# Kernel optimization log

Measured on AMD Instinct MI355X. Metric: run time of the kernel, lower is better.

Reference implementation:

```python
import jax, jax.numpy as jnp
import numpy as np


def _layernorm(x, g, b, eps=1e-5):
    mu = jnp.mean(x, axis=-1, keepdims=True)
    var = jnp.var(x, axis=-1, keepdims=True)
    return (x - mu) * jax.lax.rsqrt(var + eps) * g + b


def _forward(x_real, x_imag, dt, conv_w, conv_b, spec_re, spec_im, lam_re, lam_im,
             dt_param, sigma, noise_r, noise_i, ln_g, ln_b, W1, b1, w2, b2,
             Jg_W, Jg_b, Rg_W, Rg_b):
    B, T, C, H, W = x_real.shape
    x = x_real + 1j * x_imag  # complex field [B,T,C,H,W]

    # ---- spatial mixer: 3x3 conv applied to real/imag parts (linear op) ----
    def conv(z):
        z2 = z.reshape(B * T, C, H, W)
        y = jax.lax.conv_general_dilated(z2, conv_w, (1, 1), 'SAME',
                                         dimension_numbers=('NCHW', 'OIHW', 'NCHW'))
        return (y + conv_b[None, :, None, None]).reshape(B, T, C, H, W)
    x = x + (conv(x.real) + 1j * conv(x.imag))

    # ---- spectral mixer: pointwise complex filter in FFT domain ----
    Xf = jnp.fft.fft2(x, axes=(-2, -1), norm='ortho')
    filt = (spec_re + 1j * spec_im)[None, None]  # [1,1,C,H,W]
    x = x + jnp.fft.ifft2(Xf * filt, axes=(-2, -1), norm='ortho')

    # ---- metriplectic propagator: diagonal SSM scan in rfft2 space ----
    dt_eff = dt * jax.nn.softplus(dt_param)          # [C]
    dt_scalar = dt_eff.mean()
    xs = jnp.concatenate([x.real, x.imag], axis=0)   # [2B,T,C,H,W]; B_out=2B
    u = jnp.fft.rfft2(xs, axes=(-2, -1), norm='ortho')  # [2B,T,C,H,Wf]
    lam = -jax.nn.softplus(lam_re) + 1j * lam_im     # stable poles, [C]
    A = jnp.exp(lam * dt_eff.astype(jnp.complex64))  # [C]
    A = jnp.broadcast_to(A[None, None, :, None, None], u.shape)

    def comb(e1, e2):  # first-order linear recurrence h_t = a_t h_{t-1} + u_t
        a1, u1 = e1
        a2, u2 = e2
        return (a1 * a2, a2 * u1 + u2)
    _, h = jax.lax.associative_scan(comb, (A, u), axis=1)

    xt = jnp.fft.irfft2(h, s=(H, W), axes=(-2, -1), norm='ortho')  # [2B,T,C,H,W] real
    x_temporal = xt[:B] + 1j * xt[B:]

    noise = (noise_r + 1j * noise_i) * sigma * jnp.sqrt(dt_scalar)
    x = x + x_temporal + noise

    # ---- Port-Hamiltonian layer on real||imag channel concat ----
    xp = jnp.transpose(x, (0, 1, 3, 4, 2))                  # [B,T,H,W,C]
    xc = jnp.concatenate([xp.real, xp.imag], axis=-1)       # [B,T,H,W,2C]
    D = 2 * C
    x_in = _layernorm(xc, ln_g, ln_b)
    # grads of potential H = sum(MLP(x_in)) wrt x_in
    pot = lambda z: (jax.nn.silu(z @ W1 + b1) @ w2 + b2).sum()
    grads = jax.grad(pot)(x_in)
    M = (x_in @ Jg_W + Jg_b).reshape(*xc.shape[:-1], D, D)
    Jm = M - jnp.swapaxes(M, -1, -2)
    P = (x_in @ Rg_W + Rg_b).reshape(*xc.shape[:-1], D, D)
    R = jnp.einsum('...ki,...kj->...ij', P, P) + 1e-4 * jnp.eye(D, dtype=xc.dtype)
    update = jnp.einsum('...ij,...j->...i', Jm - R, grads)
    x_ph = xc + update * dt_scalar

    # output: [B,T,2C,H,W]; real half = out.real, imag half = out.imag
    return jnp.transpose(x_ph, (0, 1, 4, 2, 3))


def setup_inputs() -> dict:
    key = jax.random.key(0)
    ks = jax.random.split(key, 16)
    B, T, C, H, W = 2, 8, 16, 64, 64
    D = 2 * C
    hid = D * 4
    f32 = jnp.float32
    rn = lambda k, s, sc=1.0: jax.random.normal(k, s, f32) * sc
    return dict(
        x_real=rn(ks[0], (B, T, C, H, W)),
        x_imag=rn(ks[1], (B, T, C, H, W)),
        dt=jnp.asarray(0.1, f32),
        conv_w=rn(ks[2], (C, C, 3, 3), 0.05),
        conv_b=jnp.zeros((C,), f32),
        spec_re=rn(ks[3], (C, H, W), 0.1),
        spec_im=rn(ks[4], (C, H, W), 0.1),
        lam_re=rn(ks[5], (C,)),
        lam_im=rn(ks[6], (C,)),
        dt_param=rn(ks[7], (C,)),
        sigma=jnp.asarray(0.01, f32),
        noise_r=rn(ks[8], (B, T, C, H, W)),
        noise_i=rn(ks[9], (B, T, C, H, W)),
        ln_g=jnp.ones((D,), f32),
        ln_b=jnp.zeros((D,), f32),
        W1=rn(ks[10], (D, hid), 0.1),
        b1=jnp.zeros((hid,), f32),
        w2=rn(ks[11], (hid,), 0.1),
        b2=jnp.asarray(0.0, f32),
        Jg_W=rn(ks[12], (D, D * D), 0.02),
        Jg_b=jnp.zeros((D * D,), f32),
        Rg_W=rn(ks[13], (D, D * D), 0.02),
        Rg_b=jnp.zeros((D * D,), f32),
    )


def reference(x_real, x_imag, dt, conv_w, conv_b, spec_re, spec_im, lam_re, lam_im,
              dt_param, sigma, noise_r, noise_i, ln_g, ln_b, W1, b1, w2, b2,
              Jg_W, Jg_b, Rg_W, Rg_b):
    return _forward(x_real, x_imag, dt, conv_w, conv_b, spec_re, spec_im, lam_re,
                    lam_im, dt_param, sigma, noise_r, noise_i, ln_g, ln_b, W1, b1,
                    w2, b2, Jg_W, Jg_b, Rg_W, Rg_b)
```

## Files before the change

### kernel.cpp

```cpp
#include <hip/hip_runtime.h>
#include <math.h>

#define Bb 2
#define Tt 8
#define Cc 16
#define Hh 64
#define Ww 64
#define Dd 32
#define HID 128
#define NPIX 4096
#define NIMG 256

typedef unsigned short ushort_t;
typedef unsigned int uint_t;
typedef __attribute__((ext_vector_type(8))) short short8;
typedef __attribute__((ext_vector_type(4))) float f32x4;
union U16 { uint4 u; short8 s; };

__device__ __forceinline__ float sp_f(float x) {
    return (x > 20.f) ? x : log1pf(expf(x));
}

__device__ __forceinline__ ushort_t f2bf(float f) {
    uint_t u = __float_as_uint(f);
    uint_t r = (u + 0x7fffu + ((u >> 16) & 1u)) >> 16;
    return (ushort_t)r;
}
__device__ __forceinline__ float bf2f(ushort_t h) { return __uint_as_float(((uint_t)h) << 16); }

__device__ __forceinline__ uint_t packbf(float hi, float lo) {
    return __builtin_amdgcn_perm(__float_as_uint(hi), __float_as_uint(lo), 0x07060302u);
}
__device__ __forceinline__ uint4 synth8(const float* gf, float xs) {
    uint4 r;
    r.x = packbf(gf[1] * xs, gf[0] * xs);
    r.y = packbf(gf[3] * xs, gf[2] * xs);
    r.z = packbf(gf[5] * xs, gf[4] * xs);
    r.w = packbf(gf[7] * xs, gf[6] * xs);
    return r;
}
__device__ __forceinline__ void expand8(uint4 v, float* f) {
    f[0] = __uint_as_float(v.x << 16); f[1] = __uint_as_float(v.x & 0xffff0000u);
    f[2] = __uint_as_float(v.y << 16); f[3] = __uint_as_float(v.y & 0xffff0000u);
    f[4] = __uint_as_float(v.z << 16); f[5] = __uint_as_float(v.z & 0xffff0000u);
    f[6] = __uint_as_float(v.w << 16); f[7] = __uint_as_float(v.w & 0xffff0000u);
}

#define MFMA16(a, b, c) __builtin_amdgcn_mfma_f32_16x16x32_bf16((a), (b), (c), 0, 0, 0)

struct cpx { float r, i; };
__device__ __forceinline__ cpx cadd(cpx a, cpx b) { return {a.r + b.r, a.i + b.i}; }
__device__ __forceinline__ cpx csub(cpx a, cpx b) { return {a.r - b.r, a.i - b.i}; }
__device__ __forceinline__ cpx cmulw(cpx a, float wr, float wi) {
    return {a.r * wr - a.i * wi, a.r * wi + a.i * wr};
}
template<int S>
__device__ __forceinline__ cpx cmulSi(cpx a) {
    return {-(float)S * a.i, (float)S * a.r};
}
template<int S>
__device__ __forceinline__ void dft8(cpx* y) {
    const float C = 0.70710678118654752f;
    cpx t0 = cadd(y[0], y[4]), t1 = csub(y[0], y[4]);
    cpx t2 = cadd(y[2], y[6]), t3 = csub(y[2], y[6]);
    cpx e0 = cadd(t0, t2), e2 = csub(t0, t2);
    cpx t3i = cmulSi<S>(t3);
    cpx e1 = cadd(t1, t3i), e3 = csub(t1, t3i);
    cpx u0 = cadd(y[1], y[5]), u1 = csub(y[1], y[5]);
    cpx u2 = cadd(y[3], y[7]), u3 = csub(y[3], y[7]);
    cpx o0 = cadd(u0, u2), o2 = csub(u0, u2);
    cpx u3i = cmulSi<S>(u3);
    cpx o1 = cadd(u1, u3i), o3 = csub(u1, u3i);
    o1 = cmulw(o1, C, (float)S * C);
    o2 = cmulSi<S>(o2);
    o3 = cmulw(o3, -C, (float)S * C);
    y[0] = cadd(e0, o0); y[4] = csub(e0, o0);
    y[1] = cadd(e1, o1); y[5] = csub(e1, o1);
    y[2] = cadd(e2, o2); y[6] = csub(e2, o2);
    y[3] = cadd(e3, o3); y[7] = csub(e3, o3);
}

template<int S>
__device__ __forceinline__ void fft2d_r8(float* reM, float* imM,
                                         const float* twr, const float* twi, int tid) {
    int j = tid & 63, g = tid >> 6;
    {
        cpx y[8];
        #pragma unroll
        for (int n1 = 0; n1 < 8; ++n1) {
            int a = j * 65 + n1 * 8 + g;
            y[n1] = {reM[a], imM[a]};
        }
        dft8<S>(y);
        #pragma unroll
        for (int k1 = 0; k1 < 8; ++k1) {
            int m = (g * k1) & 63;
            cpx b = cmulw(y[k1], twr[m], twi[m]);
            int a = j * 65 + k1 * 8 + g;
            reM[a] = b.r; imM[a] = b.i;
        }
    }
    __syncthreads();
    {
        cpx y[8];
        #pragma unroll
        for (int n2 = 0; n2 < 8; ++n2) {
            int a = j * 65 + g * 8 + n2;
            y[n2] = {reM[a], imM[a]};
        }
        dft8<S>(y);
        __syncthreads();
        #pragma unroll
        for (int k2 = 0; k2 < 8; ++k2) {
            int a = j * 65 + g + k2 * 8;
            reM[a] = y[k2].r; imM[a] = y[k2].i;
        }
    }
    __syncthreads();
    {
        cpx y[8];
        #pragma unroll
        for (int n1 = 0; n1 < 8; ++n1) {
            int a = (n1 * 8 + g) * 65 + j;
            y[n1] = {reM[a], imM[a]};
        }
        dft8<S>(y);
        #pragma unroll
        for (int k1 = 0; k1 < 8; ++k1) {
            int m = (g * k1) & 63;
            cpx b = cmulw(y[k1], twr[m], twi[m]);
            int a = (k1 * 8 + g) * 65 + j;
            reM[a] = b.r; imM[a] = b.i;
        }
    }
    __syncthreads();
    {
        cpx y[8];
        #pragma unroll
        for (int n2 = 0; n2 < 8; ++n2) {
            int a = (g * 8 + n2) * 65 + j;
            y[n2] = {reM[a], imM[a]};
        }
        dft8<S>(y);
        __syncthreads();
        #pragma unroll
        for (int k2 = 0; k2 < 8; ++k2) {
            int a = (g + k2 * 8) * 65 + j;
            reM[a] = y[k2].r; imM[a] = y[k2].i;
        }
    }
    __syncthreads();
}

__global__ __launch_bounds__(256)
void k_conv(const float* __restrict__ xr, const float* __restrict__ xi,
            const float* __restrict__ cw, const float* __restrict__ cb,
            float2* __restrict__ x1,
            const float* __restrict__ JW, const float* __restrict__ Jb,
            const float* __restrict__ RW, const float* __restrict__ Rb,
            const float* __restrict__ W1, const float* __restrict__ dtp,
            const float* __restrict__ dt_param,
            ushort_t* __restrict__ B1f, ushort_t* __restrict__ B2f,
            ushort_t* __restrict__ w1n, ushort_t* __restrict__ w1t,
            float* __restrict__ dts_out) {
    __shared__ float sre[Cc][18][18];
    __shared__ float sim[Cc][18][18];
    __shared__ float swt[8 * 16 * 12];
    __shared__ float sb[8];
    int tid = threadIdx.x;
    if (blockIdx.x >= 512) {
        const int N1 = 33 * 3072, N2 = 33 * 1024, N3 = 4096;
        int i = (blockIdx.x - 512) * 256 + tid;
        for (; i < N1 + N2 + N3; i += 40 * 256) {
            if (i < N1) {
                int s = i / 3072; int r = i % 3072;
                int ch = r >> 9; int lane = (r >> 3) & 63; int e = i & 7;
                int n = ch * 16 + (lane & 15);
                int k = s * 32 + ((lane >> 4) << 3) + e;
                float v;
                if (k < 1024) {
                    int d = k >> 5, rr = k & 31;
                    if (n < 32)      v = JW[d * 1024 + n * 32 + rr];
                    else if (n < 64) v = JW[d * 1024 + rr * 32 + (n - 32)];
                    else             v = RW[d * 1024 + (n - 64) * 32 + rr];
                } else {
                    int rr = k - 1024;
                    if (n < 32)      v = Jb[n * 32 + rr];
                    else if (n < 64) v = Jb[rr * 32 + (n - 32)];
                    else             v = Rb[(n - 64) * 32 + rr];
                }
                B1f[i] = f2bf(v);
            } else if (i < N1 + N2) {
                int i2 = i - N1;
                int s = i2 / 1024; int r = i2 % 1024;
                int ch = r >> 9; int lane = (r >> 3) & 63; int e = i2 & 7;
                int n = ch * 16 + (lane & 15);
                int k = s * 32 + ((lane >> 4) << 3) + e;
                float v;
                if (k < 1024) {
                    int d = k >> 5, kk = k & 31;
                    v = RW[d * 1024 + kk * 32 + n];
                } else {
                    v = Rb[(k - 1024) * 32 + n];
                }
                B2f[i2] = f2bf(v);
            } else {
                int i3 = i - N1 - N2;
                int d = i3 >> 7, h = i3 & 127;
                ushort_t v = f2bf(W1[i3]);
                w1n[i3] = v;
                w1t[h * 32 + d] = v;
            }
        }
        if (blockIdx.x == 512 && tid == 0) {
            float s = 0.f;
            for (int c = 0; c < Cc; ++c) s += sp_f(dt_param[c]);
            dts_out[0] = dtp[0] * s * (1.f / Cc);
        }
        return;
    }
    int blk = blockIdx.x;
    int bt = blk >> 5;
    int sub = blk & 31;
    int tile = sub >> 1, cohalf = sub & 1;
    int ty0 = (tile >> 2) * 16, tx0 = (tile & 3) * 16;
    for (int i = tid; i < 8 * 16 * 9; i += 256) {
        int g = i / 9, k = i % 9;
        swt[g * 12 + k] = cw[cohalf * 8 * 144 + i];
    }
    if (tid < 8) sb[tid] = cb[cohalf * 8 + tid];
    for (int i = tid; i < Cc * 18 * 18; i += 256) {
        int ci = i / 324; int r = i % 324; int y = r / 18, x = r % 18;
        int gy = ty0 + y - 1, gx = tx0 + x - 1;
        float vr = 0.f, vi = 0.f;
        if (gy >= 0 && gy < Hh && gx >= 0 && gx < Ww) {
            int gidx = (bt * Cc + ci) * NPIX + gy * Ww + gx;
            vr = xr[gidx]; vi = xi[gidx];
        }
        sre[ci][y][x] = vr; sim[ci][y][x] = vi;
    }
    __syncthreads();
    int py = tid >> 4, px = tid & 15;
    int gy = ty0 + py, gx = tx0 + px;
    float ar[8], ai[8];
    #pragma unroll
    for (int oc = 0; oc < 8; ++oc) {
        int cg = cohalf * 8 + oc;
        ar[oc] = sre[cg][py + 1][px + 1] + sb[oc];
        ai[oc] = sim[cg][py + 1][px + 1] + sb[oc];
    }
    for (int ci = 0; ci < Cc; ++ci) {
        float nr[9], ni[9];
        #pragma unroll
        for (int dy = 0; dy < 3; ++dy)
            #pragma unroll
            for (int dx = 0; dx < 3; ++dx) {
                nr[dy * 3 + dx] = sre[ci][py + dy][px + dx];
                ni[dy * 3 + dx] = sim[ci][py + dy][px + dx];
            }
        #pragma unroll
        for (int oc = 0; oc < 8; ++oc) {
            const float* wp = &swt[(oc * 16 + ci) * 12];
            float4 w0 = *(const float4*)&wp[0];
            float4 w1 = *(const float4*)&wp[4];
            float w8 = wp[8];
            ar[oc] += w0.x * nr[0] + w0.y * nr[1] + w0.z * nr[2]
                    + w0.w * nr[3] + w1.x * nr[4] + w1.y * nr[5]
                    + w1.z * nr[6] + w1.w * nr[7] + w8 * nr[8];
            ai[oc] += w0.x * ni[0] + w0.y * ni[1] + w0.z * ni[2]
                    + w0.w * ni[3] + w1.x * ni[4] + w1.y * ni[5]
                    + w1.z * ni[6] + w1.w * ni[7] + w8 * ni[8];
        }
    }
    #pragma unroll
    for (int oc = 0; oc < 8; ++oc)
        x1[(bt * Cc + cohalf * 8 + oc) * NPIX + gy * Ww + gx] = make_float2(ar[oc], ai[oc]);
}

__global__ __launch_bounds__(512)
void k_fft_fwd(const float2* __restrict__ x1,
               const float* __restrict__ spec_re, const float* __restrict__ spec_im,
               float2* __restrict__ X2f) {
    int img = blockIdx.x;
    int c = img % Cc;
    int tid = threadIdx.x;
    __shared__ float re[64 * 65], im[64 * 65];
    __shared__ float twr[64], twi[64];
    if (tid < 64) {
        float ang = -0.098174770424681038798f * (float)tid;
        twr[tid] = cosf(ang); twi[tid] = sinf(ang);
    }
    const float2* src = x1 + (size_t)img * NPIX;
    for (int idx = tid; idx < NPIX; idx += 512) {
        int h = idx >> 6, w = idx & 63;
        float2 v = src[idx];
        re[h * 65 + w] = v.x; im[h * 65 + w] = v.y;
    }
    __syncthreads();
    fft2d_r8<-1>(re, im, twr, twi, tid);
    const float* fr = spec_re + c * NPIX;
    const float* fi = spec_im + c * NPIX;
    float2* dst = X2f + (size_t)img * NPIX;
    for (int idx = tid; idx < NPIX; idx += 512) {
        int h = idx >> 6, w = idx & 63;
        float xr_ = re[h * 65 + w], xi_ = im[h * 65 + w];
        float gr = 1.f + fr[idx], gi = fi[idx];
        dst[idx] = make_float2(xr_ * gr - xi_ * gi, xi_ * gr + xr_ * gi);
    }
}

__global__ __launch_bounds__(256)
void k_scan2(const float2* __restrict__ Z,
             const float* __restrict__ lam_re, const float* __restrict__ lam_im,
             const float* __restrict__ dt_param, const float* __restrict__ dtp,
             float2* __restrict__ S) {
    int id = blockIdx.x * 256 + threadIdx.x;
    int w = id & 63;
    int c = (id >> 12) & 15;
    int b = id >> 16;
    float dte = dtp[0] * sp_f(dt_param[c]);
    float ea = expf(-sp_f(lam_re[c]) * dte);
    float ph = lam_im[c] * dte;
    float Ar = ea * cosf(ph), Ai = ea * sinf(ph);
    if (w > 32) Ai = -Ai;
    bool sc = (w == 0) || (w == 32);
    int pix = id & (NPIX - 1);
    int base = (b * Tt * Cc + c) * NPIX + pix;
    float s1r = 0.f, s1i = 0.f, s2r = 0.f, s2i = 0.f;
    #pragma unroll
    for (int t = 0; t < Tt; ++t) {
        int idx = base + t * (Cc * NPIX);
        float2 zv = Z[idx];
        float nr = Ar * s1r - Ai * s1i + zv.x;
        float ni = Ar * s1i + Ai * s1r + zv.y;
        s1r = nr; s1i = ni;
        float zr, zi;
        if (sc) {
            nr = Ar * s2r + Ai * s2i + zv.x;
            ni = Ar * s2i - Ai * s2r + zv.y;
            s2r = nr; s2i = ni;
            zr = 0.5f * (s1r + s2r); zi = 0.5f * (s1i + s2i);
        } else { zr = s1r; zi = s1i; }
        S[idx] = make_float2(zv.x + zr, zv.y + zi);
    }
}

__global__ __launch_bounds__(512)
void k_fft_inv(const float2* __restrict__ Sp,
               const float* __restrict__ noise_r, const float* __restrict__ noise_i,
               const float* __restrict__ sigma_p, const float* __restrict__ dts_p,
               float2* __restrict__ xf) {
    int img = blockIdx.x; int tid = threadIdx.x;
    __shared__ float re[64 * 65], im[64 * 65];
    __shared__ float twr[64], twi[64];
    if (tid < 64) {
        float ang = 0.098174770424681038798f * (float)tid;
        twr[tid] = cosf(ang); twi[tid] = sinf(ang);
    }
    const float2* src = Sp + (size_t)img * NPIX;
    for (int idx = tid; idx < NPIX; idx += 512) {
        int h = idx >> 6, w = idx & 63;
        float2 v = src[idx];
        re[h * 65 + w] = v.x; im[h * 65 + w] = v.y;
    }
    __syncthreads();
    fft2d_r8<1>(re, im, twr, twi, tid);
    float ns = sigma_p[0] * sqrtf(dts_p[0]);
    const float inv = 1.f / 4096.f;
    float2* dst = xf + (size_t)img * NPIX;
    const float* nr = noise_r + (size_t)img * NPIX;
    const float* ni = noise_i + (size_t)img * NPIX;
    for (int idx = tid; idx < NPIX; idx += 512) {
        int h = idx >> 6, w = idx & 63;
        dst[idx] = make_float2(re[h * 65 + w] * inv + ns * nr[idx],
                               im[h * 65 + w] * inv + ns * ni[idx]);
    }
}

__global__ __launch_bounds__(256, 2)
void k_ph(const float2* __restrict__ field,
          const float* __restrict__ ln_g, const float* __restrict__ ln_b,
          const float* __restrict__ b1, const float* __restrict__ w2,
          const ushort_t* __restrict__ w1n, const ushort_t* __restrict__ w1t,
          const ushort_t* __restrict__ B1f, const ushort_t* __restrict__ B2f,
          const float* __restrict__ dts_p,
          float* __restrict__ out) {
    __shared__ ushort_t xin_s[128 * 40];
    __shared__ ushort_t g_s[128 * 40];
    __shared__ ushort_t pg_s[128 * 40];
    __shared__ ushort_t A_s[128 * 136];

    int tid = threadIdx.x;
    int bt = blockIdx.x >> 5;
    int pix0 = (blockIdx.x & 31) << 7;

    int p = tid & 127, half = tid >> 7;
    const float2* fbase = field + ((size_t)bt * 16) * NPIX + pix0 + p;
    float2 xv[8];
    float s1 = 0.f, s2 = 0.f;
    #pragma unroll
    for (int j = 0; j < 8; ++j) {
        xv[j] = fbase[(half * 8 + j) * NPIX];
        s1 += xv[j].x + xv[j].y;
        s2 += xv[j].x * xv[j].x + xv[j].y * xv[j].y;
    }
    float2* red = (float2*)A_s;
    red[p * 2 + half] = make_float2(s1, s2);
    __syncthreads();
    float2 r0 = red[p * 2], r1 = red[p * 2 + 1];
    float mu = (r0.x + r1.x) * 0.03125f;
    float var = (r0.y + r1.y) * 0.03125f - mu * mu;
    float rs = rsqrtf(var + 1e-5f);
    #pragma unroll
    for (int j = 0; j < 8; ++j) {
        int cf = half * 8 + j;
        xin_s[p * 40 + cf]      = f2bf((xv[j].x - mu) * rs * ln_g[cf] + ln_b[cf]);
        xin_s[p * 40 + cf + 16] = f2bf((xv[j].y - mu) * rs * ln_g[cf + 16] + ln_b[cf + 16]);
    }
    __syncthreads();

    int lane = tid & 63, wv = tid >> 6;
    int quad = lane >> 4, l15 = lane & 15;
    const f32x4 zero4 = {0.f, 0.f, 0.f, 0.f};

    int m0z = wv * 32;
    f32x4 zacc[2][8];
    #pragma unroll
    for (int mt = 0; mt < 2; ++mt)
        #pragma unroll
        for (int nt = 0; nt < 8; ++nt) zacc[mt][nt] = zero4;
    U16 az[2];
    #pragma unroll
    for (int mt = 0; mt < 2; ++mt)
        az[mt].u = *(const uint4*)&xin_s[(m0z + mt * 16 + l15) * 40 + quad * 8];
    #pragma unroll
    for (int nt = 0; nt < 8; ++nt) {
        U16 bz;
        bz.u = *(const uint4*)&w1t[(nt * 16 + l15) * 32 + quad * 8];
        zacc[0][nt] = MFMA16(az[0].s, bz.s, zacc[0][nt]);
        zacc[1][nt] = MFMA16(az[1].s, bz.s, zacc[1][nt]);
    }
    #pragma unroll
    for (int nt = 0; nt < 8; ++nt) {
        int col = nt * 16 + l15;
        float b1v = b1[col], w2v = w2[col];
        #pragma unroll
        for (int mt = 0; mt < 2; ++mt) {
            #pragma unroll
            for (int r = 0; r < 4; ++r) {
                int row = m0z + mt * 16 + quad * 4 + r;
                float z = zacc[mt][nt][r] + b1v;
                float s = 1.f / (1.f + expf(-z));
                float t = s * (1.f + z * (1.f - s)) * w2v;
                A_s[row * 136 + col] = f2bf(t);
            }
        }
    }

    f32x4 gacc[2][2];
    #pragma unroll
    for (int mt = 0; mt < 2; ++mt)
        #pragma unroll
        for (int nt = 0; nt < 2; ++nt) gacc[mt][nt] = zero4;
    #pragma unroll
    for (int q = 0; q < 4; ++q) {
        U16 ag[2];
        #pragma unroll
        for (int mt = 0; mt < 2; ++mt)
            ag[mt].u = *(const uint4*)&A_s[(m0z + mt * 16 + l15) * 136 + q * 32 + quad * 8];
        #pragma unroll
        for (int nt = 0; nt < 2; ++nt) {
            U16 bg;
            bg.u = *(const uint4*)&w1n[(nt * 16 + l15) * 128 + q * 32 + quad * 8];
            gacc[0][nt] = MFMA16(ag[0].s, bg.s, gacc[0][nt]);
            gacc[1][nt] = MFMA16(ag[1].s, bg.s, gacc[1][nt]);
        }
    }
    #pragma unroll
    for (int mt = 0; mt < 2; ++mt)
        #pragma unroll
        for (int nt = 0; nt < 2; ++nt)
            #pragma unroll
            for (int r = 0; r < 4; ++r)
                g_s[(m0z + mt * 16 + quad * 4 + r) * 40 + nt * 16 + l15] = f2bf(gacc[mt][nt][r]);
    __syncthreads();

    int mh = wv & 1, nh = wv >> 1;
    const uint4* B1v = (const uint4*)B1f;
    const uint4* B2v = (const uint4*)B2f;
    uint_t xw[4][16];
    uint4 gvp[4];
    float gf[4][8];
    #pragma unroll
    for (int mt = 0; mt < 4; ++mt) {
        int row = mh * 64 + mt * 16 + l15;
        #pragma unroll
        for (int q = 0; q < 4; ++q)
            *(uint4*)&xw[mt][q * 4] = *(const uint4*)&xin_s[row * 40 + q * 8];
        gvp[mt] = *(const uint4*)&g_s[row * 40 + quad * 8];
        expand8(gvp[mt], gf[mt]);
    }

    uint4 br[2][3];
    #pragma unroll
    for (int pf = 0; pf < 2; ++pf)
        #pragma unroll
        for (int jj = 0; jj < 3; ++jj)
            br[pf][jj] = B1v[(pf * 6 + nh + 2 * jj) * 64 + lane];
    f32x4 acc1[3][4];
    #pragma unroll
    for (int j = 0; j < 3; ++j)
        #pragma unroll
        for (int mt = 0; mt < 4; ++mt) acc1[j][mt] = zero4;
    #pragma unroll
    for (int s = 0; s < 33; ++s) {
        int cur = s & 1;
        U16 b3[3];
        b3[0].u = br[cur][0]; b3[1].u = br[cur][1]; b3[2].u = br[cur][2];
        #pragma unroll
        for (int mt = 0; mt < 4; ++mt) {
            U16 a;
            if (s < 32) {
                uint_t u = xw[mt][s >> 1];
                float xs = (s & 1) ? __uint_as_float(u & 0xffff0000u)
                                   : __uint_as_float(u << 16);
                a.u = synth8(gf[mt], xs);
            } else {
                a.u = gvp[mt];
            }
            acc1[0][mt] = MFMA16(a.s, b3[0].s, acc1[0][mt]);
            acc1[1][mt] = MFMA16(a.s, b3[1].s, acc1[1][mt]);
            acc1[2][mt] = MFMA16(a.s, b3[2].s, acc1[2][mt]);
        }
        if (s + 2 < 33) {
            #pragma unroll
            for (int jj = 0; jj < 3; ++jj)
                br[cur][jj] = B1v[((s + 2) * 6 + nh + 2 * jj) * 64 + lane];
        }
    }
    f32x4 um[4];
    #pragma unroll
    for (int mt = 0; mt < 4; ++mt) {
        um[mt] = acc1[0][mt] - acc1[1][mt];
        #pragma unroll
        for (int r = 0; r < 4; ++r)
            pg_s[(mh * 64 + mt * 16 + quad * 4 + r) * 40 + nh * 16 + l15] = f2bf(acc1[2][mt][r]);
    }
    __syncthreads();

    uint4 pgp[4];
    float pgf[4][8];
    #pragma unroll
    for (int mt = 0; mt < 4; ++mt) {
        int row = mh * 64 + mt * 16 + l15;
        pgp[mt] = *(const uint4*)&pg_s[row * 40 + quad * 8];
        expand8(pgp[mt], pgf[mt]);
    }
    uint4 br2[2];
    br2[0] = B2v[(0 * 2 + nh) * 64 + lane];
    br2[1] = B2v[(1 * 2 + nh) * 64 + lane];
    f32x4 acc2[4];
    #pragma unroll
    for (int mt = 0; mt < 4; ++mt) acc2[mt] = zero4;
    #pragma unroll
    for (int s = 0; s < 33; ++s) {
        int cur = s & 1;
        U16 b;
        b.u = br2[cur];
        #pragma unroll
        for (int mt = 0; mt < 4; ++mt) {
            U16 a;
            if (s < 32) {
                uint_t u = xw[mt][s >> 1];
                float xs = (s & 1) ? __uint_as_float(u & 0xffff0000u)
                                   : __uint_as_float(u << 16);
                a.u = synth8(pgf[mt], xs);
            } else {
                a.u = pgp[mt];
            }
            acc2[mt] = MFMA16(a.s, b.s, acc2[mt]);
        }
        if (s + 2 < 33)
            br2[cur] = B2v[((s + 2) * 2 + nh) * 64 + lane];
    }

    __syncthreads();
    float* upd = (float*)&A_s[8192];
    #pragma unroll
    for (int mt = 0; mt < 4; ++mt) {
        int col = nh * 16 + l15;
        #pragma unroll
        for (int r = 0; r < 4; ++r) {
            int row = mh * 64 + mt * 16 + quad * 4 + r;
            float gval = bf2f(g_s[row * 40 + col]);
            upd[row * 33 + col] = um[mt][r] - acc2[mt][r] - 1e-4f * gval;
        }
    }
    __syncthreads();
    float dts = dts_p[0];
    #pragma unroll
    for (int cc = 0; cc < 16; ++cc) {
        int c = half * 16 + cc;
        float2 v = fbase[cc * NPIX];
        float xcv = half ? v.y : v.x;
        out[((size_t)bt * 32 + c) * NPIX + pix0 + p] = xcv + dts * upd[p * 33 + c];
    }
}

extern "C" void kernel_launch(void* const* d_in, const int* in_sizes, int n_in,
                              void* d_out, int out_size, void* d_ws, size_t ws_size,
                              hipStream_t stream) {
    const float* x_real   = (const float*)d_in[0];
    const float* x_imag   = (const float*)d_in[1];
    const float* dt       = (const float*)d_in[2];
    const float* conv_w   = (const float*)d_in[3];
    const float* conv_b   = (const float*)d_in[4];
    const float* spec_re  = (const float*)d_in[5];
    const float* spec_im  = (const float*)d_in[6];
    const float* lam_re   = (const float*)d_in[7];
    const float* lam_im   = (const float*)d_in[8];
    const float* dt_param = (const float*)d_in[9];
    const float* sigma    = (const float*)d_in[10];
    const float* noise_r  = (const float*)d_in[11];
    const float* noise_i  = (const float*)d_in[12];
    const float* ln_g     = (const float*)d_in[13];
    const float* ln_b     = (const float*)d_in[14];
    const float* W1       = (const float*)d_in[15];
    const float* b1       = (const float*)d_in[16];
    const float* w2       = (const float*)d_in[17];
    const float* Jg_W     = (const float*)d_in[19];
    const float* Jg_b     = (const float*)d_in[20];
    const float* Rg_W     = (const float*)d_in[21];
    const float* Rg_b     = (const float*)d_in[22];

    float2* wsA = (float2*)d_ws;
    float2* wsB = wsA + 1048576;
    float2* wsS = wsB + 1048576;

    ushort_t* B1f = (ushort_t*)(wsS + 1048576);
    ushort_t* B2f = B1f + 33 * 3072;
    ushort_t* w1n = B2f + 33 * 1024;
    ushort_t* w1t = w1n + 4096;
    float*    dts = (float*)(w1t + 4096);

    k_conv<<<552, 256, 0, stream>>>(x_real, x_imag, conv_w, conv_b, wsA,
                                    Jg_W, Jg_b, Rg_W, Rg_b, W1, dt, dt_param,
                                    B1f, B2f, w1n, w1t, dts);
    k_fft_fwd<<<NIMG, 512, 0, stream>>>(wsA, spec_re, spec_im, wsB);
    k_scan2<<<512, 256, 0, stream>>>(wsB, lam_re, lam_im, dt_param, dt, wsS);
    k_fft_inv<<<NIMG, 512, 0, stream>>>(wsS, noise_r, noise_i, sigma, dts, wsA);
    k_ph<<<512, 256, 0, stream>>>(wsA, ln_g, ln_b, b1, w2, w1n, w1t, B1f, B2f, dts,
                                  (float*)d_out);
}
```

Measured before the change: 201.0 us.

## Repartition PH bilinear GEMMs so each wave owns rows and all output columns

Changes the work split in the port-Hamiltonian kernel's bilinear MFMA stages. Each wave now owns 32 pixel rows and computes all six B1 column chunks (and both B2 chunks), where before a 2x2 split gave each wave 64 rows and half the columns. The A-operand synthesis per wave is halved, x values are read per step from LDS instead of held in a large register array, and the compile-time unroll is done with an integer_sequence helper. The cost is that every wave streams the full B1/B2 weights from global memory, doubling weight traffic per wave. An added barrier after the A_s writes makes the reuse of shared memory safe.

```diff
diff --git a/kernel.cpp b/kernel.cpp
--- a/kernel.cpp
+++ b/kernel.cpp
@@ -1,5 +1,6 @@
 #include <hip/hip_runtime.h>
 #include <math.h>
+#include <utility>
 
 #define Bb 2
 #define Tt 8
@@ -44,6 +45,15 @@
     f[2] = __uint_as_float(v.y << 16); f[3] = __uint_as_float(v.y & 0xffff0000u);
     f[4] = __uint_as_float(v.z << 16); f[5] = __uint_as_float(v.z & 0xffff0000u);
     f[6] = __uint_as_float(v.w << 16); f[7] = __uint_as_float(v.w & 0xffff0000u);
+}
+
+template <typename F, int... Is>
+__device__ __forceinline__ void unroll_impl(F&& f, std::integer_sequence<int, Is...>) {
+    (f(std::integral_constant<int, Is>{}), ...);
+}
+template <int N, typename F>
+__device__ __forceinline__ void cunroll(F&& f) {
+    unroll_impl(f, std::make_integer_sequence<int, N>{});
 }
 
 #define MFMA16(a, b, c) __builtin_amdgcn_mfma_f32_16x16x32_bf16((a), (b), (c), 0, 0, 0)
@@ -388,7 +398,7 @@
     __shared__ ushort_t xin_s[128 * 40];
     __shared__ ushort_t g_s[128 * 40];
     __shared__ ushort_t pg_s[128 * 40];
-    __shared__ ushort_t A_s[128 * 136];
+    __shared__ ushort_t A_s[128 * 136] __attribute__((aligned(16)));
 
     int tid = threadIdx.x;
     int bt = blockIdx.x >> 5;
@@ -422,8 +432,8 @@
     int lane = tid & 63, wv = tid >> 6;
     int quad = lane >> 4, l15 = lane & 15;
     const f32x4 zero4 = {0.f, 0.f, 0.f, 0.f};
-
-    int m0z = wv * 32;
+    int m0 = wv * 32;
+
     f32x4 zacc[2][8];
     #pragma unroll
     for (int mt = 0; mt < 2; ++mt)
@@ -432,7 +442,7 @@
     U16 az[2];
     #pragma unroll
     for (int mt = 0; mt < 2; ++mt)
-        az[mt].u = *(const uint4*)&xin_s[(m0z + mt * 16 + l15) * 40 + quad * 8];
+        az[mt].u = *(const uint4*)&xin_s[(m0 + mt * 16 + l15) * 40 + quad * 8];
     #pragma unroll
     for (int nt = 0; nt < 8; ++nt) {
         U16 bz;
@@ -448,7 +458,7 @@
         for (int mt = 0; mt < 2; ++mt) {
             #pragma unroll
             for (int r = 0; r < 4; ++r) {
-                int row = m0z + mt * 16 + quad * 4 + r;
+                int row = m0 + mt * 16 + quad * 4 + r;
                 float z = zacc[mt][nt][r] + b1v;
                 float s = 1.f / (1.f + expf(-z));
                 float t = s * (1.f + z * (1.f - s)) * w2v;
@@ -456,6 +466,7 @@
             }
         }
     }
+    __syncthreads();
 
     f32x4 gacc[2][2];
     #pragma unroll
@@ -467,7 +478,7 @@
         U16 ag[2];
         #pragma unroll
         for (int mt = 0; mt < 2; ++mt)
-            ag[mt].u = *(const uint4*)&A_s[(m0z + mt * 16 + l15) * 136 + q * 32 + quad * 8];
+            ag[mt].u = *(const uint4*)&A_s[(m0 + mt * 16 + l15) * 136 + q * 32 + quad * 8];
         #pragma unroll
         for (int nt = 0; nt < 2; ++nt) {
             U16 bg;
@@ -482,118 +493,113 @@
         for (int nt = 0; nt < 2; ++nt)
             #pragma unroll
             for (int r = 0; r < 4; ++r)
-                g_s[(m0z + mt * 16 + quad * 4 + r) * 40 + nt * 16 + l15] = f2bf(gacc[mt][nt][r]);
-    __syncthreads();
-
-    int mh = wv & 1, nh = wv >> 1;
+                g_s[(m0 + mt * 16 + quad * 4 + r) * 40 + nt * 16 + l15] = f2bf(gacc[mt][nt][r]);
+    __syncthreads();
+
+    const ushort_t* xr0 = &xin_s[(m0 + l15) * 40];
+    const ushort_t* xr1 = &xin_s[(m0 + 16 + l15) * 40];
+    uint4 gvp0 = *(const uint4*)&g_s[(m0 + l15) * 40 + quad * 8];
+    uint4 gvp1 = *(const uint4*)&g_s[(m0 + 16 + l15) * 40 + quad * 8];
+    float gf0[8], gf1[8];
+    expand8(gvp0, gf0);
+    expand8(gvp1, gf1);
     const uint4* B1v = (const uint4*)B1f;
     const uint4* B2v = (const uint4*)B2f;
-    uint_t xw[4][16];
-    uint4 gvp[4];
-    float gf[4][8];
-    #pragma unroll
-    for (int mt = 0; mt < 4; ++mt) {
-        int row = mh * 64 + mt * 16 + l15;
-        #pragma unroll
-        for (int q = 0; q < 4; ++q)
-            *(uint4*)&xw[mt][q * 4] = *(const uint4*)&xin_s[row * 40 + q * 8];
-        gvp[mt] = *(const uint4*)&g_s[row * 40 + quad * 8];
-        expand8(gvp[mt], gf[mt]);
-    }
-
-    uint4 br[2][3];
+
+    uint4 br[2][6];
     #pragma unroll
     for (int pf = 0; pf < 2; ++pf)
         #pragma unroll
-        for (int jj = 0; jj < 3; ++jj)
-            br[pf][jj] = B1v[(pf * 6 + nh + 2 * jj) * 64 + lane];
-    f32x4 acc1[3][4];
-    #pragma unroll
-    for (int j = 0; j < 3; ++j)
-        #pragma unroll
-        for (int mt = 0; mt < 4; ++mt) acc1[j][mt] = zero4;
-    #pragma unroll
-    for (int s = 0; s < 33; ++s) {
-        int cur = s & 1;
-        U16 b3[3];
-        b3[0].u = br[cur][0]; b3[1].u = br[cur][1]; b3[2].u = br[cur][2];
-        #pragma unroll
-        for (int mt = 0; mt < 4; ++mt) {
-            U16 a;
-            if (s < 32) {
-                uint_t u = xw[mt][s >> 1];
-                float xs = (s & 1) ? __uint_as_float(u & 0xffff0000u)
-                                   : __uint_as_float(u << 16);
-                a.u = synth8(gf[mt], xs);
-            } else {
-                a.u = gvp[mt];
+        for (int ch = 0; ch < 6; ++ch)
+            br[pf][ch] = B1v[(pf * 6 + ch) * 64 + lane];
+    f32x4 acc1[6][2];
+    #pragma unroll
+    for (int ch = 0; ch < 6; ++ch) { acc1[ch][0] = zero4; acc1[ch][1] = zero4; }
+    cunroll<33>([&](auto Sc) {
+        constexpr int s = Sc.value;
+        constexpr int cur = s & 1;
+        U16 a0, a1;
+        if constexpr (s < 32) {
+            float x0 = bf2f(xr0[s]);
+            float x1 = bf2f(xr1[s]);
+            a0.u = synth8(gf0, x0);
+            a1.u = synth8(gf1, x1);
+        } else {
+            a0.u = gvp0; a1.u = gvp1;
+        }
+        #pragma unroll
+        for (int ch = 0; ch < 6; ++ch) {
+            U16 b; b.u = br[cur][ch];
+            acc1[ch][0] = MFMA16(a0.s, b.s, acc1[ch][0]);
+            acc1[ch][1] = MFMA16(a1.s, b.s, acc1[ch][1]);
+        }
+        if constexpr (s + 2 < 33) {
+            #pragma unroll
+            for (int ch = 0; ch < 6; ++ch)
+                br[cur][ch] = B1v[((s + 2) * 6 + ch) * 64 + lane];
+        }
+    });
+    #pragma unroll
+    for (int mt = 0; mt < 2; ++mt)
+        #pragma unroll
+        for (int c2 = 0; c2 < 2; ++c2)
+            #pragma unroll
+            for (int r = 0; r < 4; ++r)
+                pg_s[(m0 + mt * 16 + quad * 4 + r) * 40 + c2 * 16 + l15] =
+                    f2bf(acc1[4 + c2][mt][r]);
+    __syncthreads();
+
+    uint4 pgp0 = *(const uint4*)&pg_s[(m0 + l15) * 40 + quad * 8];
+    uint4 pgp1 = *(const uint4*)&pg_s[(m0 + 16 + l15) * 40 + quad * 8];
+    float pgf0[8], pgf1[8];
+    expand8(pgp0, pgf0);
+    expand8(pgp1, pgf1);
+    uint4 br2[2][2];
+    #pragma unroll
+    for (int pf = 0; pf < 2; ++pf) {
+        br2[pf][0] = B2v[(pf * 2 + 0) * 64 + lane];
+        br2[pf][1] = B2v[(pf * 2 + 1) * 64 + lane];
+    }
+    f32x4 acc2[2][2];
+    acc2[0][0] = zero4; acc2[0][1] = zero4; acc2[1][0] = zero4; acc2[1][1] = zero4;
+    cunroll<33>([&](auto Sc) {
+        constexpr int s = Sc.value;
+        constexpr int cur = s & 1;
+        U16 a0, a1;
+        if constexpr (s < 32) {
+            float x0 = bf2f(xr0[s]);
+            float x1 = bf2f(xr1[s]);
+            a0.u = synth8(pgf0, x0);
+            a1.u = synth8(pgf1, x1);
+        } else {
+            a0.u = pgp0; a1.u = pgp1;
+        }
+        #pragma unroll
+        for (int ch = 0; ch < 2; ++ch) {
+            U16 b; b.u = br2[cur][ch];
+            acc2[ch][0] = MFMA16(a0.s, b.s, acc2[ch][0]);
+            acc2[ch][1] = MFMA16(a1.s, b.s, acc2[ch][1]);
+        }
+        if constexpr (s + 2 < 33) {
+            br2[cur][0] = B2v[((s + 2) * 2 + 0) * 64 + lane];
+            br2[cur][1] = B2v[((s + 2) * 2 + 1) * 64 + lane];
+        }
+    });
+
+    __syncthreads();
+    float* upd = (float*)A_s;
+    #pragma unroll
+    for (int mt = 0; mt < 2; ++mt) {
+        #pragma unroll
+        for (int c2 = 0; c2 < 2; ++c2) {
+            int col = c2 * 16 + l15;
+            #pragma unroll
+            for (int r = 0; r < 4; ++r) {
+                int row = m0 + mt * 16 + quad * 4 + r;
+                float gval = bf2f(g_s[row * 40 + col]);
+                upd[row * 33 + col] = (acc1[c2][mt][r] - acc1[c2 + 2][mt][r])
+                                      - acc2[c2][mt][r] - 1e-4f * gval;
             }
-            acc1[0][mt] = MFMA16(a.s, b3[0].s, acc1[0][mt]);
-            acc1[1][mt] = MFMA16(a.s, b3[1].s, acc1[1][mt]);
-            acc1[2][mt] = MFMA16(a.s, b3[2].s, acc1[2][mt]);
-        }
-        if (s + 2 < 33) {
-            #pragma unroll
-            for (int jj = 0; jj < 3; ++jj)
-                br[cur][jj] = B1v[((s + 2) * 6 + nh + 2 * jj) * 64 + lane];
-        }
-    }
-    f32x4 um[4];
-    #pragma unroll
-    for (int mt = 0; mt < 4; ++mt) {
-        um[mt] = acc1[0][mt] - acc1[1][mt];
-        #pragma unroll
-        for (int r = 0; r < 4; ++r)
-            pg_s[(mh * 64 + mt * 16 + quad * 4 + r) * 40 + nh * 16 + l15] = f2bf(acc1[2][mt][r]);
-    }
-    __syncthreads();
-
-    uint4 pgp[4];
-    float pgf[4][8];
-    #pragma unroll
-    for (int mt = 0; mt < 4; ++mt) {
-        int row = mh * 64 + mt * 16 + l15;
-        pgp[mt] = *(const uint4*)&pg_s[row * 40 + quad * 8];
-        expand8(pgp[mt], pgf[mt]);
-    }
-    uint4 br2[2];
-    br2[0] = B2v[(0 * 2 + nh) * 64 + lane];
-    br2[1] = B2v[(1 * 2 + nh) * 64 + lane];
-    f32x4 acc2[4];
-    #pragma unroll
-    for (int mt = 0; mt < 4; ++mt) acc2[mt] = zero4;
-    #pragma unroll
-    for (int s = 0; s < 33; ++s) {
-        int cur = s & 1;
-        U16 b;
-        b.u = br2[cur];
-        #pragma unroll
-        for (int mt = 0; mt < 4; ++mt) {
-            U16 a;
-            if (s < 32) {
-                uint_t u = xw[mt][s >> 1];
-                float xs = (s & 1) ? __uint_as_float(u & 0xffff0000u)
-                                   : __uint_as_float(u << 16);
-                a.u = synth8(pgf[mt], xs);
-            } else {
-                a.u = pgp[mt];
-            }
-            acc2[mt] = MFMA16(a.s, b.s, acc2[mt]);
-        }
-        if (s + 2 < 33)
-            br2[cur] = B2v[((s + 2) * 2 + nh) * 64 + lane];
-    }
-
-    __syncthreads();
-    float* upd = (float*)&A_s[8192];
-    #pragma unroll
-    for (int mt = 0; mt < 4; ++mt) {
-        int col = nh * 16 + l15;
-        #pragma unroll
-        for (int r = 0; r < 4; ++r) {
-            int row = mh * 64 + mt * 16 + quad * 4 + r;
-            float gval = bf2f(g_s[row * 40 + col]);
-            upd[row * 33 + col] = um[mt][r] - acc2[mt][r] - 1e-4f * gval;
         }
     }
     __syncthreads();
```

Result: faster. 189.4 us (-5.8%).
